# Kernel tuning notes

Measured on AMD Instinct MI355X. Metric: run time of the kernel, lower is better.

## Reference

```python
import jax, jax.numpy as jnp
import numpy as np

T = 8192        # minority samples
D = 128         # n_hidden (SMOTE dims)
K = 3           # smote k
N_MULT = 4      # synthetic samples per minority row (N/100)
C = 16          # n_classes


def setup_inputs() -> dict:
    key = jax.random.key(0)
    k1, k2, k3, k4 = jax.random.split(key, 4)
    X = jax.random.normal(k1, (T, D), dtype=jnp.float32)
    # randint(0, k-2) inclusive in torch -> values in {0, ..., K-2}
    nn_idx = jax.random.randint(k2, (N_MULT * T,), 0, K - 1, dtype=jnp.int32)
    gaps = jax.random.uniform(k3, (N_MULT * T,), dtype=jnp.float32)
    W = jax.random.normal(k4, (D, C), dtype=jnp.float32) / np.float32(np.sqrt(D))
    b = jnp.zeros((C,), dtype=jnp.float32)
    return {"X": X, "nn_idx": nn_idx, "gaps": gaps, "W": W, "b": b}


def reference(X, nn_idx, gaps, W, b):
    # --- find_k: full pairwise euclidean distance (fused, replaces per-row loop) ---
    sq = jnp.sum(X * X, axis=1)                       # [T]
    d2 = sq[:, None] + sq[None, :] - 2.0 * (X @ X.T)  # [T, T]
    dist = jnp.sqrt(jnp.maximum(d2, 0.0))
    # --- k_neighbors: k smallest distances; col 0 is self (dist 0) ---
    _, idxs = jax.lax.top_k(-dist, K)                 # [T, K], ascending distance
    nbrs = idxs[:, 1:K]                               # [T, K-1]
    # --- populate: gather-based interpolation, N_MULT synthetic rows per source ---
    src = jnp.repeat(jnp.arange(T), N_MULT)           # [N_syn], row order matches torch loop
    chosen = nbrs[src, nn_idx]                        # [N_syn]
    x_src = X[src]                                    # [N_syn, D]
    syn = x_src + gaps[:, None] * (X[chosen] - x_src) # [N_syn, D]
    # --- classifier on concatenated real + synthetic embeddings ---
    Xa = jnp.concatenate([X, syn], axis=0)            # [T + N_syn, D]
    logits = Xa @ W + b                               # [T + N_syn, C]
    return logits
```

## Files before the change

### kernel.cpp

```cpp
#include <hip/hip_runtime.h>

#define T_PTS 8192
#define D_DIM 128
#define C_OUT 16
#define NSPLIT 8
#define JSPAN (T_PTS / NSPLIT)
#define NJT (JSPAN / 64)
#define LSTR 132

typedef _Float16 half8 __attribute__((ext_vector_type(8)));
typedef __attribute__((ext_vector_type(4))) float f32x4;
typedef unsigned short ushort_t;
typedef unsigned int uint_t;


__global__ void prep_kernel(const float* __restrict__ X, _Float16* __restrict__ Xs,
                            float* __restrict__ sq) {
    const int tid = threadIdx.x;
    const int row = blockIdx.x * 16 + (tid >> 4);
    const int ch = tid & 15;
    const float4* p = (const float4*)(X + row * D_DIM + ch * 8);
    const float4 a = p[0], b = p[1];
    half8 o;
    o[0] = (_Float16)a.x; o[1] = (_Float16)a.y; o[2] = (_Float16)a.z; o[3] = (_Float16)a.w;
    o[4] = (_Float16)b.x; o[5] = (_Float16)b.y; o[6] = (_Float16)b.z; o[7] = (_Float16)b.w;
    const int t = row >> 4, m = row & 15, k = ch >> 2, q = ch & 3;
    *(half8*)(Xs + t * 2048 + k * 512 + (q * 16 + m) * 8) = o;
    float s = a.x * a.x + a.y * a.y + a.z * a.z + a.w * a.w
            + b.x * b.x + b.y * b.y + b.z * b.z + b.w * b.w;
    s += __shfl_xor(s, 1); s += __shfl_xor(s, 2);
    s += __shfl_xor(s, 4); s += __shfl_xor(s, 8);
    if (ch == 0) sq[row] = s;
}

#define INS4(c0_, c1_, c2_, c3_, v_)                         \
    do {                                                     \
        const float _v = (v_);                               \
        c3_ = __builtin_amdgcn_fmed3f(c2_, c3_, _v);         \
        c2_ = __builtin_amdgcn_fmed3f(c1_, c2_, _v);         \
        c1_ = __builtin_amdgcn_fmed3f(c0_, c1_, _v);         \
        c0_ = fminf(c0_, _v);                                \
    } while (0)

__launch_bounds__(256, 2)
__global__ void nn_kernel(const _Float16* __restrict__ Xs, const float* __restrict__ sq,
                          float* __restrict__ ckey, ushort_t* __restrict__ cidx) {
    __shared__ float mkLds[4][64][5];

    const int tid = threadIdx.x;
    const int w = tid >> 6;
    const int lane = tid & 63;
    const int quad = lane >> 4;
    const int l15 = lane & 15;
    const int i0 = blockIdx.x * 64;
    const int sp = blockIdx.y;
    const int j0 = sp * JSPAN;

    half8 bfrag[4][4];
#pragma unroll
    for (int n = 0; n < 4; ++n)
#pragma unroll
        for (int k = 0; k < 4; ++k)
            bfrag[n][k] = *(const half8*)(Xs + ((i0 >> 4) + n) * 2048 + k * 512 + lane * 8);

    float c0[4], c1[4], c2[4], c3[4], sk[4];
#pragma unroll
    for (int n = 0; n < 4; ++n) { c0[n] = c1[n] = c2[n] = c3[n] = sk[n] = 1e30f; }

    const bool blk_excl = (sp == (i0 / JSPAN));
    const int excl_jt = (i0 & (JSPAN - 1)) >> 6;

    half8 af[4];
    f32x4 sq4;
    {
        const int jtile = (j0 >> 4) + w;
#pragma unroll
        for (int k = 0; k < 4; ++k)
            af[k] = *(const half8*)(Xs + jtile * 2048 + k * 512 + lane * 8);
        sq4 = *(const f32x4*)(sq + j0 + w * 16 + quad * 4);
    }

#pragma unroll 2
    for (int jt = 0; jt < NJT; ++jt) {
        const int jbase = j0 + jt * 64;
        const int jg = jbase + w * 16 + quad * 4;
        half8 afn[4];
        f32x4 sq4n;
        {
            const int jb2 = j0 + ((jt + 1) & (NJT - 1)) * 64;
            const int jtile2 = (jb2 >> 4) + w;
#pragma unroll
            for (int k = 0; k < 4; ++k)
                afn[k] = *(const half8*)(Xs + jtile2 * 2048 + k * 512 + lane * 8);
            sq4n = *(const f32x4*)(sq + jb2 + w * 16 + quad * 4);
        }
        const bool excl = blk_excl && (jt == excl_jt);
        const uint_t ib = (uint_t)((quad << 6) | (jt * 4));

#pragma unroll
        for (int n = 0; n < 4; ++n) {
            f32x4 acc = {0.f, 0.f, 0.f, 0.f};
#pragma unroll
            for (int k = 0; k < 4; ++k)
                acc = __builtin_amdgcn_mfma_f32_16x16x32_f16(af[k], bfrag[n][k], acc, 0, 0, 0);
            float q0 = fmaf(-2.f, acc[0], sq4[0]);
            float q1 = fmaf(-2.f, acc[1], sq4[1]);
            float q2 = fmaf(-2.f, acc[2], sq4[2]);
            float q3 = fmaf(-2.f, acc[3], sq4[3]);
            if (excl) {
                const int ic = i0 + n * 16 + l15;
                if (jg + 0 == ic) q0 = 1e30f;
                if (jg + 1 == ic) q1 = 1e30f;
                if (jg + 2 == ic) q2 = 1e30f;
                if (jg + 3 == ic) q3 = 1e30f;
            }
            const float p0 = __uint_as_float((__float_as_uint(q0) & 0xFFFFFF00u) | (ib + 0));
            const float p1 = __uint_as_float((__float_as_uint(q1) & 0xFFFFFF00u) | (ib + 1));
            const float p2 = __uint_as_float((__float_as_uint(q2) & 0xFFFFFF00u) | (ib + 2));
            const float p3 = __uint_as_float((__float_as_uint(q3) & 0xFFFFFF00u) | (ib + 3));
            const float min01 = fminf(p0, p1), max01 = fmaxf(p0, p1);
            const float min23 = fminf(p2, p3), max23 = fmaxf(p2, p3);
            const float kmin = fminf(min01, min23);
            const float ksec = fminf(fmaxf(min01, min23), fminf(max01, max23));
            INS4(c0[n], c1[n], c2[n], c3[n], kmin);
            sk[n] = fminf(sk[n], ksec);
        }
#pragma unroll
        for (int k = 0; k < 4; ++k) af[k] = afn[k];
        sq4 = sq4n;
    }

#pragma unroll
    for (int n = 0; n < 4; ++n) {
        INS4(c0[n], c1[n], c2[n], c3[n], sk[n]);
        float d0 = __shfl_xor(c0[n], 16), d1 = __shfl_xor(c1[n], 16);
        float d2 = __shfl_xor(c2[n], 16), d3 = __shfl_xor(c3[n], 16);
        INS4(c0[n], c1[n], c2[n], c3[n], d0);
        INS4(c0[n], c1[n], c2[n], c3[n], d1);
        INS4(c0[n], c1[n], c2[n], c3[n], d2);
        INS4(c0[n], c1[n], c2[n], c3[n], d3);
        d0 = __shfl_xor(c0[n], 32); d1 = __shfl_xor(c1[n], 32);
        d2 = __shfl_xor(c2[n], 32); d3 = __shfl_xor(c3[n], 32);
        INS4(c0[n], c1[n], c2[n], c3[n], d0);
        INS4(c0[n], c1[n], c2[n], c3[n], d1);
        INS4(c0[n], c1[n], c2[n], c3[n], d2);
        INS4(c0[n], c1[n], c2[n], c3[n], d3);
    }

    if (quad == 0) {
#pragma unroll
        for (int n = 0; n < 4; ++n) {
            const int row = n * 16 + l15;
            mkLds[w][row][0] = c0[n];
            mkLds[w][row][1] = c1[n];
            mkLds[w][row][2] = c2[n];
            mkLds[w][row][3] = c3[n];
        }
    }
    __syncthreads();
    if (tid < 64) {
        float a0 = 1e30f, a1 = 1e30f, a2 = 1e30f, a3 = 1e30f;
        int b0 = 0, b1 = 0, b2 = 0, b3 = 0;
#pragma unroll
        for (int wv = 0; wv < 4; ++wv)
#pragma unroll
            for (int e = 0; e < 4; ++e) {
                const float kk = mkLds[wv][tid][e];
                const uint_t p8 = __float_as_uint(kk) & 255u;
                const int j = j0 + (int)((p8 & 63u) >> 2) * 64 + wv * 16
                            + (int)((p8 >> 6) & 3u) * 4 + (int)(p8 & 3u);
                bool l0 = kk < a0, l1 = kk < a1, l2 = kk < a2, l3 = kk < a3;
                a3 = l2 ? a2 : (l3 ? kk : a3); b3 = l2 ? b2 : (l3 ? j : b3);
                a2 = l1 ? a1 : (l2 ? kk : a2); b2 = l1 ? b1 : (l2 ? j : b2);
                a1 = l0 ? a0 : (l1 ? kk : a1); b1 = l0 ? b0 : (l1 ? j : b1);
                a0 = l0 ? kk : a0;             b0 = l0 ? j : b0;
            }
        const int gi = i0 + tid;
        f32x4 kv = {a0, a1, a2, a3};
        *(f32x4*)(ckey + (sp * T_PTS + gi) * 4) = kv;
        ushort_t* c = cidx + (sp * T_PTS + gi) * 4;
        c[0] = (ushort_t)b0; c[1] = (ushort_t)b1; c[2] = (ushort_t)b2; c[3] = (ushort_t)b3;
    }
}

__global__ void tail_kernel(const float* __restrict__ X, const float* __restrict__ sq,
                            const float* __restrict__ ckey, const ushort_t* __restrict__ cidx,
                            int* __restrict__ nbrs) {
    __shared__ ushort_t cLds[32][33];
    __shared__ ushort_t nb8s[32][8];
    __shared__ float keys[32][9];
    __shared__ int idxs[32][9];
    const int tid = threadIdx.x;
    const int ib0 = blockIdx.x * 32;

    if (tid < 32) {
        const int i = ib0 + tid;
        float c0 = 1e30f, c1 = 1e30f, c2 = 1e30f, c3 = 1e30f;
        float c4 = 1e30f, c5 = 1e30f, c6 = 1e30f, c7 = 1e30f;
#pragma unroll
        for (int sp2 = 0; sp2 < NSPLIT; ++sp2) {
            const f32x4 kk = *(const f32x4*)(ckey + (sp2 * T_PTS + i) * 4);
            ushort_t j4[4];
            *(uint2*)j4 = *(const uint2*)(cidx + (sp2 * T_PTS + i) * 4);
#pragma unroll
            for (int e4 = 0; e4 < 4; ++e4) {
                const uint_t e = (uint_t)(sp2 * 4 + e4);
                const float v = __uint_as_float((__float_as_uint(kk[e4]) & 0xFFFFFFC0u) | e);
                cLds[tid][e] = j4[e4];
                c7 = __builtin_amdgcn_fmed3f(c6, c7, v);
                c6 = __builtin_amdgcn_fmed3f(c5, c6, v);
                c5 = __builtin_amdgcn_fmed3f(c4, c5, v);
                c4 = __builtin_amdgcn_fmed3f(c3, c4, v);
                c3 = __builtin_amdgcn_fmed3f(c2, c3, v);
                c2 = __builtin_amdgcn_fmed3f(c1, c2, v);
                c1 = __builtin_amdgcn_fmed3f(c0, c1, v);
                c0 = fminf(c0, v);
            }
        }
        const float top[8] = {c0, c1, c2, c3, c4, c5, c6, c7};
#pragma unroll
        for (int r = 0; r < 8; ++r)
            nb8s[tid][r] = cLds[tid][__float_as_uint(top[r]) & 63u];
    }
    __syncthreads();
    {
        const int rr = tid >> 3, cc = tid & 7;
        const int i = ib0 + rr;
        const int j = (int)nb8s[rr][cc];
        const float4* xi = (const float4*)(X + i * D_DIM);
        const float4* xj = (const float4*)(X + j * D_DIM);
        float ssum = 0.f;
#pragma unroll
        for (int q = 0; q < 32; ++q) {
            const float4 a = xi[q], b2 = xj[q];
            ssum += a.x * b2.x; ssum += a.y * b2.y; ssum += a.z * b2.z; ssum += a.w * b2.w;
        }
        float key = sq[j] - 2.f * ssum;
        if (j == i) key = 1e30f;
        keys[rr][cc] = key;
        idxs[rr][cc] = j;
    }
    __syncthreads();
    if (tid < 32) {
        float m0 = 1e30f, m1 = 1e30f;
        int n0 = 0x7fffffff, n1 = 0x7fffffff;
#pragma unroll
        for (int e = 0; e < 8; ++e) {
            const float k = keys[tid][e];
            const int j = idxs[tid][e];
            bool lt0 = (k < m0) || (k == m0 && j < n0);
            bool lt1 = (k < m1) || (k == m1 && j < n1);
            if (lt0) { m1 = m0; n1 = n0; m0 = k; n0 = j; }
            else if (lt1) { m1 = k; n1 = j; }
        }
        const int i = ib0 + tid;
        nbrs[i * 2 + 0] = n0;
        nbrs[i * 2 + 1] = n1;
    }
}

__launch_bounds__(256)
__global__ void y_kernel(const float* __restrict__ X, const float* __restrict__ W,
                         const float* __restrict__ b, float* __restrict__ Y,
                         float* __restrict__ out) {
    __shared__ float Xsl[16 * LSTR];
    __shared__ float Ws[D_DIM * C_OUT];
    const int tid = threadIdx.x;
    const int r0 = blockIdx.x * 16;
    const float4* src = (const float4*)(X + r0 * D_DIM);
#pragma unroll
    for (int it = 0; it < 2; ++it) {
        int f = tid + it * 256;
        int row = f >> 5, kq = f & 31;
        *(float4*)(Xsl + row * LSTR + kq * 4) = src[row * 32 + kq];
    }
#pragma unroll
    for (int it = 0; it < 2; ++it) {
        int f = tid + it * 256;
        ((float4*)Ws)[f] = ((const float4*)W)[f];
    }
    __syncthreads();
    const int r = tid >> 4, c = tid & 15;
    float s = b[c];
#pragma unroll
    for (int d = 0; d < D_DIM; ++d) s += Xsl[r * LSTR + d] * Ws[d * C_OUT + c];
    const int row = r0 + r;
    Y[row * C_OUT + c] = s;
    out[row * C_OUT + c] = s;
}

__global__ void syn_kernel(const float* __restrict__ Y, const int* __restrict__ nbrs,
                           const int* __restrict__ nn_idx, const float* __restrict__ gaps,
                           float* __restrict__ out) {
    const int idx = blockIdx.x * 256 + threadIdx.x;
    const int m = idx >> 4;
    const int c = idx & 15;
    const int src = m >> 2;
    const int sel = nn_idx[m];
    const int ch = nbrs[src * 2 + sel];
    const float g = gaps[m];
    const float ys = Y[src * C_OUT + c];
    const float yc = Y[ch * C_OUT + c];
    out[(T_PTS + m) * C_OUT + c] = ys + g * (yc - ys);
}

extern "C" void kernel_launch(void* const* d_in, const int* in_sizes, int n_in,
                              void* d_out, int out_size, void* d_ws, size_t ws_size,
                              hipStream_t stream) {
    const float* X = (const float*)d_in[0];
    const int* nn_idx = (const int*)d_in[1];
    const float* gaps = (const float*)d_in[2];
    const float* W = (const float*)d_in[3];
    const float* b = (const float*)d_in[4];
    float* out = (float*)d_out;

    char* ws = (char*)d_ws;
    _Float16* Xs = (_Float16*)ws;
    float* sq = (float*)(ws + 2097152);
    float* ckey = (float*)(ws + 2129920);
    ushort_t* cidx = (ushort_t*)(ws + 3178496);
    int* nbrs = (int*)(ws + 3702784);
    float* Y = (float*)(ws + 2129920);

    prep_kernel<<<T_PTS / 16, 256, 0, stream>>>(X, Xs, sq);
    nn_kernel<<<dim3(T_PTS / 64, NSPLIT), 256, 0, stream>>>(Xs, sq, ckey, cidx);
    tail_kernel<<<T_PTS / 32, 256, 0, stream>>>(X, sq, ckey, cidx, nbrs);
    y_kernel<<<T_PTS / 16, 256, 0, stream>>>(X, W, b, Y, out);
    syn_kernel<<<(4 * T_PTS * C_OUT) / 256, 256, 0, stream>>>(Y, nbrs, nn_idx, gaps, out);
}
```

Baseline: 111.2 us.

## Fuse y/syn kernels into prep/tail and halve nearest-neighbor column splits

The classifier matmul (y_kernel) now runs as extra blocks of prep_kernel, and the synthetic interpolation (syn_kernel) is folded into tail_kernel using neighbor indices kept in shared memory. That cuts five launches down to three and drops the global nbrs round trip. NSPLIT goes from 8 to 4, so each nn block scans twice as many columns and tail merges fewer candidates. The packed-index bits in the key rise from 8 to 9, which costs one more mantissa bit of distance precision. The nn grid shrinks to 512 blocks, which may leave the GPU less well filled.

```diff
diff --git a/kernel.cpp b/kernel.cpp
--- a/kernel.cpp
+++ b/kernel.cpp
@@ -3,35 +3,17 @@
 #define T_PTS 8192
 #define D_DIM 128
 #define C_OUT 16
-#define NSPLIT 8
+#define NSPLIT 4
 #define JSPAN (T_PTS / NSPLIT)
 #define NJT (JSPAN / 64)
 #define LSTR 132
+#define PREP_BLOCKS (T_PTS / 16)
 
 typedef _Float16 half8 __attribute__((ext_vector_type(8)));
 typedef __attribute__((ext_vector_type(4))) float f32x4;
 typedef unsigned short ushort_t;
 typedef unsigned int uint_t;
 
-
-__global__ void prep_kernel(const float* __restrict__ X, _Float16* __restrict__ Xs,
-                            float* __restrict__ sq) {
-    const int tid = threadIdx.x;
-    const int row = blockIdx.x * 16 + (tid >> 4);
-    const int ch = tid & 15;
-    const float4* p = (const float4*)(X + row * D_DIM + ch * 8);
-    const float4 a = p[0], b = p[1];
-    half8 o;
-    o[0] = (_Float16)a.x; o[1] = (_Float16)a.y; o[2] = (_Float16)a.z; o[3] = (_Float16)a.w;
-    o[4] = (_Float16)b.x; o[5] = (_Float16)b.y; o[6] = (_Float16)b.z; o[7] = (_Float16)b.w;
-    const int t = row >> 4, m = row & 15, k = ch >> 2, q = ch & 3;
-    *(half8*)(Xs + t * 2048 + k * 512 + (q * 16 + m) * 8) = o;
-    float s = a.x * a.x + a.y * a.y + a.z * a.z + a.w * a.w
-            + b.x * b.x + b.y * b.y + b.z * b.z + b.w * b.w;
-    s += __shfl_xor(s, 1); s += __shfl_xor(s, 2);
-    s += __shfl_xor(s, 4); s += __shfl_xor(s, 8);
-    if (ch == 0) sq[row] = s;
-}
 
 #define INS4(c0_, c1_, c2_, c3_, v_)                         \
     do {                                                     \
@@ -41,6 +23,53 @@
         c1_ = __builtin_amdgcn_fmed3f(c0_, c1_, _v);         \
         c0_ = fminf(c0_, _v);                                \
     } while (0)
+
+__global__ void prep_kernel(const float* __restrict__ X, _Float16* __restrict__ Xs,
+                            float* __restrict__ sq, const float* __restrict__ W,
+                            const float* __restrict__ b, float* __restrict__ Y,
+                            float* __restrict__ out) {
+    const int tid = threadIdx.x;
+    if (blockIdx.x < PREP_BLOCKS) {
+        const int row = blockIdx.x * 16 + (tid >> 4);
+        const int ch = tid & 15;
+        const float4* p = (const float4*)(X + row * D_DIM + ch * 8);
+        const float4 a = p[0], bb = p[1];
+        half8 o;
+        o[0] = (_Float16)a.x;  o[1] = (_Float16)a.y;  o[2] = (_Float16)a.z;  o[3] = (_Float16)a.w;
+        o[4] = (_Float16)bb.x; o[5] = (_Float16)bb.y; o[6] = (_Float16)bb.z; o[7] = (_Float16)bb.w;
+        const int t = row >> 4, m = row & 15, k = ch >> 2, q = ch & 3;
+        *(half8*)(Xs + t * 2048 + k * 512 + (q * 16 + m) * 8) = o;
+        float s = a.x * a.x + a.y * a.y + a.z * a.z + a.w * a.w
+                + bb.x * bb.x + bb.y * bb.y + bb.z * bb.z + bb.w * bb.w;
+        s += __shfl_xor(s, 1); s += __shfl_xor(s, 2);
+        s += __shfl_xor(s, 4); s += __shfl_xor(s, 8);
+        if (ch == 0) sq[row] = s;
+    } else {
+        __shared__ float Xsl[16 * LSTR];
+        __shared__ float Ws[D_DIM * C_OUT];
+        const int r0 = (blockIdx.x - PREP_BLOCKS) * 16;
+        const float4* src = (const float4*)(X + r0 * D_DIM);
+#pragma unroll
+        for (int it = 0; it < 2; ++it) {
+            int f = tid + it * 256;
+            int row = f >> 5, kq = f & 31;
+            *(float4*)(Xsl + row * LSTR + kq * 4) = src[row * 32 + kq];
+        }
+#pragma unroll
+        for (int it = 0; it < 2; ++it) {
+            int f = tid + it * 256;
+            ((float4*)Ws)[f] = ((const float4*)W)[f];
+        }
+        __syncthreads();
+        const int r = tid >> 4, c = tid & 15;
+        float s = b[c];
+#pragma unroll
+        for (int d = 0; d < D_DIM; ++d) s += Xsl[r * LSTR + d] * Ws[d * C_OUT + c];
+        const int row = r0 + r;
+        Y[row * C_OUT + c] = s;
+        out[row * C_OUT + c] = s;
+    }
+}
 
 __launch_bounds__(256, 2)
 __global__ void nn_kernel(const _Float16* __restrict__ Xs, const float* __restrict__ sq,
@@ -95,7 +124,7 @@
             sq4n = *(const f32x4*)(sq + jb2 + w * 16 + quad * 4);
         }
         const bool excl = blk_excl && (jt == excl_jt);
-        const uint_t ib = (uint_t)((quad << 6) | (jt * 4));
+        const uint_t ib = (uint_t)((quad << 7) | (jt * 4));
 
 #pragma unroll
         for (int n = 0; n < 4; ++n) {
@@ -114,10 +143,10 @@
                 if (jg + 2 == ic) q2 = 1e30f;
                 if (jg + 3 == ic) q3 = 1e30f;
             }
-            const float p0 = __uint_as_float((__float_as_uint(q0) & 0xFFFFFF00u) | (ib + 0));
-            const float p1 = __uint_as_float((__float_as_uint(q1) & 0xFFFFFF00u) | (ib + 1));
-            const float p2 = __uint_as_float((__float_as_uint(q2) & 0xFFFFFF00u) | (ib + 2));
-            const float p3 = __uint_as_float((__float_as_uint(q3) & 0xFFFFFF00u) | (ib + 3));
+            const float p0 = __uint_as_float((__float_as_uint(q0) & 0xFFFFFE00u) | (ib + 0));
+            const float p1 = __uint_as_float((__float_as_uint(q1) & 0xFFFFFE00u) | (ib + 1));
+            const float p2 = __uint_as_float((__float_as_uint(q2) & 0xFFFFFE00u) | (ib + 2));
+            const float p3 = __uint_as_float((__float_as_uint(q3) & 0xFFFFFE00u) | (ib + 3));
             const float min01 = fminf(p0, p1), max01 = fmaxf(p0, p1);
             const float min23 = fminf(p2, p3), max23 = fmaxf(p2, p3);
             const float kmin = fminf(min01, min23);
@@ -166,9 +195,9 @@
 #pragma unroll
             for (int e = 0; e < 4; ++e) {
                 const float kk = mkLds[wv][tid][e];
-                const uint_t p8 = __float_as_uint(kk) & 255u;
-                const int j = j0 + (int)((p8 & 63u) >> 2) * 64 + wv * 16
-                            + (int)((p8 >> 6) & 3u) * 4 + (int)(p8 & 3u);
+                const uint_t p9 = __float_as_uint(kk) & 511u;
+                const int j = j0 + (int)((p9 & 127u) >> 2) * 64 + wv * 16
+                            + (int)(p9 >> 7) * 4 + (int)(p9 & 3u);
                 bool l0 = kk < a0, l1 = kk < a1, l2 = kk < a2, l3 = kk < a3;
                 a3 = l2 ? a2 : (l3 ? kk : a3); b3 = l2 ? b2 : (l3 ? j : b3);
                 a2 = l1 ? a1 : (l2 ? kk : a2); b2 = l1 ? b1 : (l2 ? j : b2);
@@ -185,11 +214,13 @@
 
 __global__ void tail_kernel(const float* __restrict__ X, const float* __restrict__ sq,
                             const float* __restrict__ ckey, const ushort_t* __restrict__ cidx,
-                            int* __restrict__ nbrs) {
-    __shared__ ushort_t cLds[32][33];
+                            const float* __restrict__ Y, const int* __restrict__ nn_idx,
+                            const float* __restrict__ gaps, float* __restrict__ out) {
+    __shared__ ushort_t cLds[32][17];
     __shared__ ushort_t nb8s[32][8];
     __shared__ float keys[32][9];
     __shared__ int idxs[32][9];
+    __shared__ int nbr2[32][2];
     const int tid = threadIdx.x;
     const int ib0 = blockIdx.x * 32;
 
@@ -205,7 +236,7 @@
 #pragma unroll
             for (int e4 = 0; e4 < 4; ++e4) {
                 const uint_t e = (uint_t)(sp2 * 4 + e4);
-                const float v = __uint_as_float((__float_as_uint(kk[e4]) & 0xFFFFFFC0u) | e);
+                const float v = __uint_as_float((__float_as_uint(kk[e4]) & 0xFFFFFFF0u) | e);
                 cLds[tid][e] = j4[e4];
                 c7 = __builtin_amdgcn_fmed3f(c6, c7, v);
                 c6 = __builtin_amdgcn_fmed3f(c5, c6, v);
@@ -220,7 +251,7 @@
         const float top[8] = {c0, c1, c2, c3, c4, c5, c6, c7};
 #pragma unroll
         for (int r = 0; r < 8; ++r)
-            nb8s[tid][r] = cLds[tid][__float_as_uint(top[r]) & 63u];
+            nb8s[tid][r] = cLds[tid][__float_as_uint(top[r]) & 15u];
     }
     __syncthreads();
     {
@@ -253,55 +284,26 @@
             if (lt0) { m1 = m0; n1 = n0; m0 = k; n0 = j; }
             else if (lt1) { m1 = k; n1 = j; }
         }
-        const int i = ib0 + tid;
-        nbrs[i * 2 + 0] = n0;
-        nbrs[i * 2 + 1] = n1;
-    }
-}
-
-__launch_bounds__(256)
-__global__ void y_kernel(const float* __restrict__ X, const float* __restrict__ W,
-                         const float* __restrict__ b, float* __restrict__ Y,
-                         float* __restrict__ out) {
-    __shared__ float Xsl[16 * LSTR];
-    __shared__ float Ws[D_DIM * C_OUT];
-    const int tid = threadIdx.x;
-    const int r0 = blockIdx.x * 16;
-    const float4* src = (const float4*)(X + r0 * D_DIM);
-#pragma unroll
-    for (int it = 0; it < 2; ++it) {
-        int f = tid + it * 256;
-        int row = f >> 5, kq = f & 31;
-        *(float4*)(Xsl + row * LSTR + kq * 4) = src[row * 32 + kq];
-    }
-#pragma unroll
-    for (int it = 0; it < 2; ++it) {
-        int f = tid + it * 256;
-        ((float4*)Ws)[f] = ((const float4*)W)[f];
+        nbr2[tid][0] = n0;
+        nbr2[tid][1] = n1;
     }
     __syncthreads();
-    const int r = tid >> 4, c = tid & 15;
-    float s = b[c];
-#pragma unroll
-    for (int d = 0; d < D_DIM; ++d) s += Xsl[r * LSTR + d] * Ws[d * C_OUT + c];
-    const int row = r0 + r;
-    Y[row * C_OUT + c] = s;
-    out[row * C_OUT + c] = s;
-}
-
-__global__ void syn_kernel(const float* __restrict__ Y, const int* __restrict__ nbrs,
-                           const int* __restrict__ nn_idx, const float* __restrict__ gaps,
-                           float* __restrict__ out) {
-    const int idx = blockIdx.x * 256 + threadIdx.x;
-    const int m = idx >> 4;
-    const int c = idx & 15;
-    const int src = m >> 2;
-    const int sel = nn_idx[m];
-    const int ch = nbrs[src * 2 + sel];
-    const float g = gaps[m];
-    const float ys = Y[src * C_OUT + c];
-    const float yc = Y[ch * C_OUT + c];
-    out[(T_PTS + m) * C_OUT + c] = ys + g * (yc - ys);
+    {
+        const int c = tid & 15;
+        const int g16 = tid >> 4;
+#pragma unroll
+        for (int e = 0; e < 8; ++e) {
+            const int m_local = g16 + 16 * e;
+            const int src_local = m_local >> 2;
+            const int m_global = ib0 * 4 + m_local;
+            const int sel = nn_idx[m_global];
+            const int ch = nbr2[src_local][sel];
+            const float g = gaps[m_global];
+            const float ys = Y[(ib0 + src_local) * C_OUT + c];
+            const float yc = Y[ch * C_OUT + c];
+            out[(T_PTS + m_global) * C_OUT + c] = ys + g * (yc - ys);
+        }
+    }
 }
 
 extern "C" void kernel_launch(void* const* d_in, const int* in_sizes, int n_in,
@@ -318,13 +320,10 @@
     _Float16* Xs = (_Float16*)ws;
     float* sq = (float*)(ws + 2097152);
     float* ckey = (float*)(ws + 2129920);
-    ushort_t* cidx = (ushort_t*)(ws + 3178496);
-    int* nbrs = (int*)(ws + 3702784);
-    float* Y = (float*)(ws + 2129920);
-
-    prep_kernel<<<T_PTS / 16, 256, 0, stream>>>(X, Xs, sq);
+    ushort_t* cidx = (ushort_t*)(ws + 2654208);
+    float* Y = (float*)(ws + 2916352);
+
+    prep_kernel<<<2 * PREP_BLOCKS, 256, 0, stream>>>(X, Xs, sq, W, b, Y, out);
     nn_kernel<<<dim3(T_PTS / 64, NSPLIT), 256, 0, stream>>>(Xs, sq, ckey, cidx);
-    tail_kernel<<<T_PTS / 32, 256, 0, stream>>>(X, sq, ckey, cidx, nbrs);
-    y_kernel<<<T_PTS / 16, 256, 0, stream>>>(X, W, b, Y, out);
-    syn_kernel<<<(4 * T_PTS * C_OUT) / 256, 256, 0, stream>>>(Y, nbrs, nn_idx, gaps, out);
+    tail_kernel<<<T_PTS / 32, 256, 0, stream>>>(X, sq, ckey, cidx, Y, nn_idx, gaps, out);
 }
```

Result: faster. 105.3 us (median of 2 runs) (-5.2%).
